# Performance work log

Hardware: AMD Instinct MI355X
Metric: run time of the kernel (lower is better)

## Reference

```python
import jax, jax.numpy as jnp
import numpy as np

D_MODEL = 1024
D_STATE = 32
EXPAND = 2
D_INNER = D_MODEL * EXPAND          # 2048
DT_RANK = D_MODEL // 16             # 64
LN_EPS = 1e-5


def setup_inputs() -> dict:
    key = jax.random.key(0)
    ks = jax.random.split(key, 9)
    s = 0.02
    x = jax.random.normal(ks[0], (2, 2048, D_MODEL), dtype=jnp.float32)
    W_in = jax.random.normal(ks[1], (2 * D_INNER, D_MODEL), dtype=jnp.float32) * s
    W_x = jax.random.normal(ks[2], (DT_RANK + 2 * D_STATE, D_INNER), dtype=jnp.float32) * s
    W_dt = jax.random.normal(ks[3], (D_INNER, DT_RANK), dtype=jnp.float32) * s
    b_dt = jax.random.normal(ks[4], (D_INNER,), dtype=jnp.float32) * s
    A_real0 = jax.random.normal(ks[5], (D_INNER, D_STATE), dtype=jnp.float32) * 0.5
    A_log_real = jnp.log(jnp.clip(-A_real0, 1e-4, None))
    A_imag = jax.random.normal(ks[6], (D_INNER, D_STATE), dtype=jnp.float32) * 0.1
    D_param = jnp.ones((D_INNER,), dtype=jnp.float32)
    W_out = jax.random.normal(ks[7], (D_MODEL, D_INNER), dtype=jnp.float32) * s
    ln_g = jnp.ones((D_MODEL,), dtype=jnp.float32)
    ln_b = jnp.zeros((D_MODEL,), dtype=jnp.float32)
    return {"x": x, "W_in": W_in, "W_x": W_x, "W_dt": W_dt, "b_dt": b_dt,
            "A_log_real": A_log_real, "A_imag": A_imag, "D_param": D_param,
            "W_out": W_out, "ln_g": ln_g, "ln_b": ln_b}


def _forward(x, W_in, W_x, W_dt, b_dt, A_log_real, A_imag, D_param, W_out, ln_g, ln_b):
    B, T, _ = x.shape
    residual = x
    # LayerNorm
    mu = jnp.mean(x, axis=-1, keepdims=True)
    var = jnp.mean((x - mu) ** 2, axis=-1, keepdims=True)
    xn = (x - mu) * jax.lax.rsqrt(var + LN_EPS) * ln_g + ln_b
    # in_proj -> (x_ssm, z)
    xz = jnp.einsum('btd,ed->bte', xn, W_in)            # (B,T,2*d_inner)
    x_ssm, z = jnp.split(xz, 2, axis=-1)
    # x_proj -> dt_low, B, C
    x_dbl = jnp.einsum('bte,re->btr', x_ssm, W_x)        # (B,T,dt_rank+2*d_state)
    dt_low = x_dbl[..., :DT_RANK]
    B_param = x_dbl[..., DT_RANK:DT_RANK + D_STATE]      # (B,T,N)
    C_param = x_dbl[..., DT_RANK + D_STATE:]             # (B,T,N)
    dt = jax.nn.softplus(jnp.einsum('btr,er->bte', dt_low, W_dt) + b_dt)  # (B,T,d_inner)
    # A = -exp(A_log_real) + i * A_imag, complex state split into (hr, hi)
    Ar = -jnp.exp(A_log_real)                             # (d_inner,N)
    Ai = A_imag

    def step(carry, inp):
        hr, hi = carry                                    # (B,d_inner,N)
        dt_t, B_t, C_t, x_t = inp                         # (B,d_inner),(B,N),(B,N),(B,d_inner)
        dtE = dt_t[:, :, None]                            # (B,d_inner,1)
        scale = jnp.exp(Ar[None] * dtE)
        ang = Ai[None] * dtE
        dAr = scale * jnp.cos(ang)
        dAi = scale * jnp.sin(ang)
        dBx = (dt_t * x_t)[:, :, None] * B_t[:, None, :]  # real input injection
        hr2 = dAr * hr - dAi * hi + dBx
        hi2 = dAr * hi + dAi * hr
        y = jnp.sum(hr2 * C_t[:, None, :], axis=-1)       # real part of (h * C).sum
        return (hr2, hi2), y

    h0 = jnp.zeros((B, D_INNER, D_STATE), dtype=x.dtype)
    xs = (jnp.transpose(dt, (1, 0, 2)), jnp.transpose(B_param, (1, 0, 2)),
          jnp.transpose(C_param, (1, 0, 2)), jnp.transpose(x_ssm, (1, 0, 2)))
    _, ys = jax.lax.scan(step, (h0, h0), xs)              # (T,B,d_inner)
    y = jnp.transpose(ys, (1, 0, 2)) + D_param * x_ssm
    y = y * jax.nn.silu(z)
    out = jnp.einsum('bte,de->btd', y, W_out)
    return residual + out  # dropout is identity at eval


def reference(x, W_in, W_x, W_dt, b_dt, A_log_real, A_imag, D_param, W_out, ln_g, ln_b):
    return _forward(x, W_in, W_x, W_dt, b_dt, A_log_real, A_imag, D_param, W_out, ln_g, ln_b)
```

## Files before the change

kernel.cpp:

```cpp
#include <hip/hip_runtime.h>
#include <math.h>

#define D_MODEL 1024
#define D_STATE 32
#define D_INNER 2048
#define DT_RANK 64
#define BT 4096
#define XZLD 4224
#define LN_EPS 1e-5f

typedef __attribute__((ext_vector_type(8))) short short8;
typedef __attribute__((ext_vector_type(4))) float f32x4;
typedef const __attribute__((address_space(1))) void* gp_t;
typedef __attribute__((address_space(3))) void* lp_t;

__device__ __forceinline__ ushort bf16r(float f) {
    unsigned u = __float_as_uint(f);
    u += 0x7fff + ((u >> 16) & 1);
    return (ushort)(u >> 16);
}

__global__ __launch_bounds__(256) void cvt_bf16(const float* __restrict__ in,
                                                ushort* __restrict__ out, int n4) {
    int i = blockIdx.x * 256 + threadIdx.x;
    if (i >= n4) return;
    float4 v = ((const float4*)in)[i];
    ushort4 o;
    o.x = bf16r(v.x); o.y = bf16r(v.y); o.z = bf16r(v.z); o.w = bf16r(v.w);
    ((ushort4*)out)[i] = o;
}

__global__ __launch_bounds__(256) void transpose_cvt(const float* __restrict__ in,
                                                     ushort* __restrict__ out) {
    __shared__ float tile[32][33];
    int bx = blockIdx.x * 32;
    int by = blockIdx.y * 32;
    int tx = threadIdx.x & 31, ty = threadIdx.x >> 5;
    #pragma unroll
    for (int i = 0; i < 32; i += 8)
        tile[ty + i][tx] = in[(size_t)(bx + ty + i) * 1024 + by + tx];
    __syncthreads();
    #pragma unroll
    for (int i = 0; i < 32; i += 8)
        out[(size_t)(by + ty + i) * 2048 + bx + tx] = bf16r(tile[tx][ty + i]);
}

__global__ __launch_bounds__(256) void ln_kernel(const float* __restrict__ x,
                                                 const float* __restrict__ g,
                                                 const float* __restrict__ b,
                                                 ushort* __restrict__ xn) {
    int row = blockIdx.x;
    const float4* xr = (const float4*)(x + (size_t)row * D_MODEL);
    float4 v = xr[threadIdx.x];
    float s  = v.x + v.y + v.z + v.w;
    float ss = v.x*v.x + v.y*v.y + v.z*v.z + v.w*v.w;
    #pragma unroll
    for (int off = 32; off > 0; off >>= 1) {
        s  += __shfl_down(s,  off, 64);
        ss += __shfl_down(ss, off, 64);
    }
    __shared__ float rs[4], rss[4];
    int wave = threadIdx.x >> 6;
    if ((threadIdx.x & 63) == 0) { rs[wave] = s; rss[wave] = ss; }
    __syncthreads();
    s  = rs[0] + rs[1] + rs[2] + rs[3];
    ss = rss[0] + rss[1] + rss[2] + rss[3];
    float mu  = s * (1.f / D_MODEL);
    float var = ss * (1.f / D_MODEL) - mu * mu;
    float inv = rsqrtf(var + LN_EPS);
    float4 gv = ((const float4*)g)[threadIdx.x];
    float4 bv = ((const float4*)b)[threadIdx.x];
    ushort4 o;
    o.x = bf16r((v.x - mu) * inv * gv.x + bv.x);
    o.y = bf16r((v.y - mu) * inv * gv.y + bv.y);
    o.z = bf16r((v.z - mu) * inv * gv.z + bv.z);
    o.w = bf16r((v.w - mu) * inv * gv.w + bv.w);
    ((ushort4*)(xn + (size_t)row * D_MODEL))[threadIdx.x] = o;
}

template<int RESID>
__global__ __launch_bounds__(256) void gemm_bt_bf16(
    const ushort* __restrict__ A, const ushort* __restrict__ B,
    float* __restrict__ C, int ldc, int K,
    const float* __restrict__ resid)
{
    __shared__ __align__(16) ushort As[128 * 32];
    __shared__ __align__(16) ushort Bs[128 * 32];
    int tid = threadIdx.x;
    int bm = blockIdx.x * 128, bn = blockIdx.y * 128;
    int wave = tid >> 6, lane = tid & 63;
    int wm = (wave & 1) * 64, wn = (wave >> 1) * 64;
    int quad = lane >> 4, m16 = lane & 15;
    int grow = tid >> 2;
    int gcol = (tid & 3) * 8;
    const size_t a0 = (size_t)(bm + grow) * K + gcol;
    const size_t b0 = (size_t)(bn + grow) * K + gcol;
    char* asw = (char*)As + wave * 1024;
    char* bsw = (char*)Bs + wave * 1024;

    f32x4 acc[4][4] = {};
    for (int k0 = 0; k0 < K; k0 += 32) {
        __builtin_amdgcn_global_load_lds((gp_t)(A + a0 + k0),                 (lp_t)asw,          16, 0, 0);
        __builtin_amdgcn_global_load_lds((gp_t)(A + a0 + (size_t)64*K + k0),  (lp_t)(asw + 4096), 16, 0, 0);
        __builtin_amdgcn_global_load_lds((gp_t)(B + b0 + k0),                 (lp_t)bsw,          16, 0, 0);
        __builtin_amdgcn_global_load_lds((gp_t)(B + b0 + (size_t)64*K + k0),  (lp_t)(bsw + 4096), 16, 0, 0);
        __syncthreads();
        short8 af[4], bf[4];
        #pragma unroll
        for (int i = 0; i < 4; ++i)
            af[i] = *(const short8*)&As[(wm + i * 16 + m16) * 32 + quad * 8];
        #pragma unroll
        for (int j = 0; j < 4; ++j)
            bf[j] = *(const short8*)&Bs[(wn + j * 16 + m16) * 32 + quad * 8];
        #pragma unroll
        for (int i = 0; i < 4; ++i)
            #pragma unroll
            for (int j = 0; j < 4; ++j)
                acc[i][j] = __builtin_amdgcn_mfma_f32_16x16x32_bf16(
                    af[i], bf[j], acc[i][j], 0, 0, 0);
        __syncthreads();
    }
    #pragma unroll
    for (int i = 0; i < 4; ++i) {
        #pragma unroll
        for (int r = 0; r < 4; ++r) {
            int row = bm + wm + i * 16 + quad * 4 + r;
            #pragma unroll
            for (int j = 0; j < 4; ++j) {
                int col = bn + wn + j * 16 + m16;
                float v = acc[i][j][r];
                if (RESID) v += resid[(size_t)row * ldc + col];
                C[(size_t)row * ldc + col] = v;
            }
        }
    }
}

template<int ACT>
__global__ __launch_bounds__(256) void gemm_nt(const float* __restrict__ A, int lda,
                                               const float* __restrict__ B, int ldb,
                                               float* __restrict__ C, int ldc,
                                               int K,
                                               const float* __restrict__ bias) {
    __shared__ float As[16][68];
    __shared__ float Bs[16][68];
    int tid = threadIdx.x;
    int bm = blockIdx.x * 64;
    int bn = blockIdx.y * 64;
    int tx = tid & 15, ty = tid >> 4;
    int lr = tid >> 2;
    int lk = (tid & 3) << 2;
    const float* Ap = A + (size_t)(bm + lr) * lda + lk;
    const float* Bp = B + (size_t)(bn + lr) * ldb + lk;
    float acc[4][4] = {};
    for (int k0 = 0; k0 < K; k0 += 16) {
        float4 a4 = *(const float4*)(Ap + k0);
        float4 b4 = *(const float4*)(Bp + k0);
        As[lk+0][lr] = a4.x; As[lk+1][lr] = a4.y; As[lk+2][lr] = a4.z; As[lk+3][lr] = a4.w;
        Bs[lk+0][lr] = b4.x; Bs[lk+1][lr] = b4.y; Bs[lk+2][lr] = b4.z; Bs[lk+3][lr] = b4.w;
        __syncthreads();
        #pragma unroll
        for (int k = 0; k < 16; ++k) {
            float4 av = *(const float4*)&As[k][ty << 2];
            float4 bv = *(const float4*)&Bs[k][tx << 2];
            float ar[4] = {av.x, av.y, av.z, av.w};
            float br[4] = {bv.x, bv.y, bv.z, bv.w};
            #pragma unroll
            for (int i = 0; i < 4; ++i)
                #pragma unroll
                for (int j = 0; j < 4; ++j)
                    acc[i][j] = fmaf(ar[i], br[j], acc[i][j]);
        }
        __syncthreads();
    }
    #pragma unroll
    for (int i = 0; i < 4; ++i) {
        int row = bm + (ty << 2) + i;
        #pragma unroll
        for (int j = 0; j < 4; ++j) {
            int col = bn + (tx << 2) + j;
            float v = acc[i][j];
            if (bias)  v += bias[col];
            if (ACT == 1) v = (v > 20.f) ? v : __logf(1.f + __expf(v));
            C[(size_t)row * ldc + col] = v;
        }
    }
}

__global__ __launch_bounds__(256) void scan_kernel(
    const float* __restrict__ xz,
    const float* __restrict__ dtm,
    const float* __restrict__ A_log_real,
    const float* __restrict__ A_imag,
    const float* __restrict__ D_param,
    ushort* __restrict__ y)
{
    const int tid = threadIdx.x;
    const int s   = tid & 31;
    const int el  = tid >> 5;
    const int b   = blockIdx.x >> 8;
    const int e0  = (blockIdx.x & 255) << 3;
    const int e   = e0 + el;
    const int stt = tid >> 3;
    const int sk  = tid & 7;
    const int btt = tid >> 4;
    const int bk  = (tid & 15) << 2;

    __shared__ __align__(16) float dxz[2][8][32][4];
    __shared__ __align__(16) float bcs[2][32][64];
    __shared__ __align__(16) float red[8][32][32];

    const float Ar   = -__expf(A_log_real[e * D_STATE + s]);
    const float Ai2p = A_imag[e * D_STATE + s] * 0.15915494f;
    const float Dp   = D_param[e];
    float hr = 0.f, hi = 0.f;
    const float* xzb = xz + (size_t)b * 2048 * XZLD;
    const float* bcb = xzb + 4096 + DT_RANK;
    const float* dtb = dtm + (size_t)b * 2048 * 2048;
    ushort*      yb  = y   + (size_t)b * 2048 * 2048;
    const int sx4 = (s & 7) << 2;

    float r_d, r_x, r_z;
    float4 r_bc0, r_bc1;
    {
        r_d = dtb[(size_t)stt * 2048 + e0 + sk];
        r_x = xzb[(size_t)stt * XZLD + e0 + sk];
        r_z = xzb[(size_t)stt * XZLD + 2048 + e0 + sk];
        r_bc0 = *(const float4*)&bcb[(size_t)btt * XZLD + bk];
        r_bc1 = *(const float4*)&bcb[(size_t)(btt + 16) * XZLD + bk];
        dxz[0][sk][stt][0] = r_d; dxz[0][sk][stt][2] = r_x; dxz[0][sk][stt][3] = r_z;
        *(float4*)&bcs[0][btt][bk]      = r_bc0;
        *(float4*)&bcs[0][btt + 16][bk] = r_bc1;
    }
    for (int c = 0; c < 64; ++c) {
        const int buf = c & 1;
        __syncthreads();
        if (c < 63) {
            const int tn = (c + 1) * 32;
            r_d = dtb[(size_t)(tn + stt) * 2048 + e0 + sk];
            r_x = xzb[(size_t)(tn + stt) * XZLD + e0 + sk];
            r_z = xzb[(size_t)(tn + stt) * XZLD + 2048 + e0 + sk];
            r_bc0 = *(const float4*)&bcb[(size_t)(tn + btt) * XZLD + bk];
            r_bc1 = *(const float4*)&bcb[(size_t)(tn + btt + 16) * XZLD + bk];
        }
        #pragma unroll 8
        for (int tt = 0; tt < 32; ++tt) {
            float4 dxv = *(const float4*)&dxz[buf][el][tt][0];
            float Bv = bcs[buf][tt][s];
            float Cv = bcs[buf][tt][32 + s];
            float dtv = dxv.x, xv = dxv.z;
            float sc = __expf(Ar * dtv);
            float u  = Ai2p * dtv;
            float sa = __builtin_amdgcn_sinf(u);
            float ca = __builtin_amdgcn_cosf(u);
            float dAr = sc * ca, dAi = sc * sa;
            float dBx = (dtv * xv) * Bv;
            float hr2 = dAr * hr - dAi * hi + dBx;
            hi = dAr * hi + dAi * hr;
            hr = hr2;
            red[el][tt][s ^ ((tt & 7) << 2)] = hr * Cv;
        }
        float acc = 0.f;
        #pragma unroll
        for (int p = 0; p < 8; ++p) {
            float4 v = *(const float4*)&red[el][s][(p << 2) ^ sx4];
            acc += (v.x + v.y) + (v.z + v.w);
        }
        float2 xzg = *(const float2*)&dxz[buf][el][s][2];
        float sig = 1.f / (1.f + __expf(-xzg.y));
        yb[(size_t)(c * 32 + s) * 2048 + e] = bf16r((acc + Dp * xzg.x) * xzg.y * sig);
        if (c < 63) {
            const int nb = buf ^ 1;
            dxz[nb][sk][stt][0] = r_d; dxz[nb][sk][stt][2] = r_x; dxz[nb][sk][stt][3] = r_z;
            *(float4*)&bcs[nb][btt][bk]      = r_bc0;
            *(float4*)&bcs[nb][btt + 16][bk] = r_bc1;
        }
    }
}

extern "C" void kernel_launch(void* const* d_in, const int* in_sizes, int n_in,
                              void* d_out, int out_size, void* d_ws, size_t ws_size,
                              hipStream_t stream) {
    const float* x          = (const float*)d_in[0];
    const float* W_in       = (const float*)d_in[1];
    const float* W_x        = (const float*)d_in[2];
    const float* W_dt       = (const float*)d_in[3];
    const float* b_dt       = (const float*)d_in[4];
    const float* A_log_real = (const float*)d_in[5];
    const float* A_imag     = (const float*)d_in[6];
    const float* D_param    = (const float*)d_in[7];
    const float* W_out      = (const float*)d_in[8];
    const float* ln_g       = (const float*)d_in[9];
    const float* ln_b       = (const float*)d_in[10];
    float* out = (float*)d_out;

    char* ws = (char*)d_ws;
    float*  xz      = (float*) (ws);
    float*  dt      = (float*) (ws + ((size_t) 66 << 20));
    ushort* xn_bf   = (ushort*)(ws + ((size_t) 98 << 20));
    ushort* Waug    = (ushort*)(ws + ((size_t)106 << 20));
    ushort* y_bf    = (ushort*)(ws + ((size_t)115 << 20));
    ushort* Wout_bf = (ushort*)(ws + ((size_t)131 << 20));
    float*  Wcomb   = (float*) (ws);
    ushort* Wx_bf   = (ushort*)(ws + ((size_t)  1 << 20));
    ushort* WinT_bf = (ushort*)(ws + ((size_t)  2 << 20));

    cvt_bf16<<<4096, 256, 0, stream>>>(W_in,  Waug,    4096*1024/4);
    cvt_bf16<<<2048, 256, 0, stream>>>(W_out, Wout_bf, 1024*2048/4);
    cvt_bf16<<< 256, 256, 0, stream>>>(W_x,   Wx_bf,    128*2048/4);
    transpose_cvt<<<dim3(64, 32), 256, 0, stream>>>(W_in, WinT_bf);
    gemm_bt_bf16<0><<<dim3(1, 8), 256, 0, stream>>>(
        Wx_bf, WinT_bf, Wcomb, 1024, 2048, nullptr);
    cvt_bf16<<<128, 256, 0, stream>>>(Wcomb, Waug + (size_t)4096*1024, 128*1024/4);
    ln_kernel<<<BT, 256, 0, stream>>>(x, ln_g, ln_b, xn_bf);
    gemm_bt_bf16<0><<<dim3(BT/128, XZLD/128), 256, 0, stream>>>(
        xn_bf, Waug, xz, XZLD, D_MODEL, nullptr);
    gemm_nt<1><<<dim3(BT/64, D_INNER/64), 256, 0, stream>>>(
        xz + 4096, XZLD, W_dt, DT_RANK, dt, D_INNER, DT_RANK, b_dt);
    scan_kernel<<<512, 256, 0, stream>>>(xz, dt, A_log_real, A_imag, D_param, y_bf);
    gemm_bt_bf16<1><<<dim3(BT/128, D_MODEL/128), 256, 0, stream>>>(
        y_bf, Wout_bf, out, D_MODEL, D_INNER, x);
}
```

Measured before the change: 509.7 us.

## Move dt projection to bf16 MFMA GEMM and restructure scan reduction with DPP

Replaces the fp32 scalar dt-projection GEMM with the bf16 MFMA GEMM, adding a softplus+bias epilogue, a bf16 conversion of dt_low and of W_dt. The scan kernel now precomputes dt*x, D*x and silu(z) once per chunk in shared memory. It processes two timesteps per iteration, uses exp2 with a prescaled A, and swaps the shared-memory transposed reduction over states for DPP cross-lane reductions. Extra kernel launches and bf16 rounding of dt_low add small cost and some precision loss.

```diff
diff --git a/kernel.cpp b/kernel.cpp
--- a/kernel.cpp
+++ b/kernel.cpp
@@ -20,11 +20,36 @@
     return (ushort)(u >> 16);
 }
 
+__device__ __forceinline__ float dpp_red32(float x) {
+    int t;
+    t = __builtin_amdgcn_update_dpp(0, __float_as_int(x), 0x111, 0xf, 0xf, true);
+    x += __int_as_float(t);
+    t = __builtin_amdgcn_update_dpp(0, __float_as_int(x), 0x112, 0xf, 0xf, true);
+    x += __int_as_float(t);
+    t = __builtin_amdgcn_update_dpp(0, __float_as_int(x), 0x114, 0xf, 0xf, true);
+    x += __int_as_float(t);
+    t = __builtin_amdgcn_update_dpp(0, __float_as_int(x), 0x118, 0xf, 0xf, true);
+    x += __int_as_float(t);
+    t = __builtin_amdgcn_update_dpp(0, __float_as_int(x), 0x142, 0xa, 0xf, true);
+    x += __int_as_float(t);
+    return x;
+}
+
 __global__ __launch_bounds__(256) void cvt_bf16(const float* __restrict__ in,
                                                 ushort* __restrict__ out, int n4) {
     int i = blockIdx.x * 256 + threadIdx.x;
     if (i >= n4) return;
     float4 v = ((const float4*)in)[i];
+    ushort4 o;
+    o.x = bf16r(v.x); o.y = bf16r(v.y); o.z = bf16r(v.z); o.w = bf16r(v.w);
+    ((ushort4*)out)[i] = o;
+}
+
+__global__ __launch_bounds__(256) void cvt_dtlow(const float* __restrict__ xz,
+                                                 ushort* __restrict__ out) {
+    int i = blockIdx.x * 256 + threadIdx.x;
+    int row = i >> 4, c = (i & 15) << 2;
+    float4 v = *(const float4*)&xz[(size_t)row * XZLD + 4096 + c];
     ushort4 o;
     o.x = bf16r(v.x); o.y = bf16r(v.y); o.z = bf16r(v.z); o.w = bf16r(v.w);
     ((ushort4*)out)[i] = o;
@@ -78,11 +103,11 @@
     ((ushort4*)(xn + (size_t)row * D_MODEL))[threadIdx.x] = o;
 }
 
-template<int RESID>
+template<int RESID, int ACT>
 __global__ __launch_bounds__(256) void gemm_bt_bf16(
     const ushort* __restrict__ A, const ushort* __restrict__ B,
     float* __restrict__ C, int ldc, int K,
-    const float* __restrict__ resid)
+    const float* __restrict__ resid, const float* __restrict__ bias)
 {
     __shared__ __align__(16) ushort As[128 * 32];
     __shared__ __align__(16) ushort Bs[128 * 32];
@@ -129,60 +154,13 @@
             for (int j = 0; j < 4; ++j) {
                 int col = bn + wn + j * 16 + m16;
                 float v = acc[i][j][r];
+                if (ACT == 1) {
+                    v += bias[col];
+                    v = (v > 20.f) ? v : __logf(1.f + __expf(v));
+                }
                 if (RESID) v += resid[(size_t)row * ldc + col];
                 C[(size_t)row * ldc + col] = v;
             }
-        }
-    }
-}
-
-template<int ACT>
-__global__ __launch_bounds__(256) void gemm_nt(const float* __restrict__ A, int lda,
-                                               const float* __restrict__ B, int ldb,
-                                               float* __restrict__ C, int ldc,
-                                               int K,
-                                               const float* __restrict__ bias) {
-    __shared__ float As[16][68];
-    __shared__ float Bs[16][68];
-    int tid = threadIdx.x;
-    int bm = blockIdx.x * 64;
-    int bn = blockIdx.y * 64;
-    int tx = tid & 15, ty = tid >> 4;
-    int lr = tid >> 2;
-    int lk = (tid & 3) << 2;
-    const float* Ap = A + (size_t)(bm + lr) * lda + lk;
-    const float* Bp = B + (size_t)(bn + lr) * ldb + lk;
-    float acc[4][4] = {};
-    for (int k0 = 0; k0 < K; k0 += 16) {
-        float4 a4 = *(const float4*)(Ap + k0);
-        float4 b4 = *(const float4*)(Bp + k0);
-        As[lk+0][lr] = a4.x; As[lk+1][lr] = a4.y; As[lk+2][lr] = a4.z; As[lk+3][lr] = a4.w;
-        Bs[lk+0][lr] = b4.x; Bs[lk+1][lr] = b4.y; Bs[lk+2][lr] = b4.z; Bs[lk+3][lr] = b4.w;
-        __syncthreads();
-        #pragma unroll
-        for (int k = 0; k < 16; ++k) {
-            float4 av = *(const float4*)&As[k][ty << 2];
-            float4 bv = *(const float4*)&Bs[k][tx << 2];
-            float ar[4] = {av.x, av.y, av.z, av.w};
-            float br[4] = {bv.x, bv.y, bv.z, bv.w};
-            #pragma unroll
-            for (int i = 0; i < 4; ++i)
-                #pragma unroll
-                for (int j = 0; j < 4; ++j)
-                    acc[i][j] = fmaf(ar[i], br[j], acc[i][j]);
-        }
-        __syncthreads();
-    }
-    #pragma unroll
-    for (int i = 0; i < 4; ++i) {
-        int row = bm + (ty << 2) + i;
-        #pragma unroll
-        for (int j = 0; j < 4; ++j) {
-            int col = bn + (tx << 2) + j;
-            float v = acc[i][j];
-            if (bias)  v += bias[col];
-            if (ACT == 1) v = (v > 20.f) ? v : __logf(1.f + __expf(v));
-            C[(size_t)row * ldc + col] = v;
         }
     }
 }
@@ -195,42 +173,47 @@
     const float* __restrict__ D_param,
     ushort* __restrict__ y)
 {
-    const int tid = threadIdx.x;
-    const int s   = tid & 31;
-    const int el  = tid >> 5;
-    const int b   = blockIdx.x >> 8;
-    const int e0  = (blockIdx.x & 255) << 3;
-    const int e   = e0 + el;
-    const int stt = tid >> 3;
-    const int sk  = tid & 7;
-    const int btt = tid >> 4;
-    const int bk  = (tid & 15) << 2;
-
-    __shared__ __align__(16) float dxz[2][8][32][4];
-    __shared__ __align__(16) float bcs[2][32][64];
-    __shared__ __align__(16) float red[8][32][32];
-
-    const float Ar   = -__expf(A_log_real[e * D_STATE + s]);
+    const int tid  = threadIdx.x;
+    const int s    = tid & 31;
+    const int el   = tid >> 5;
+    const int b    = blockIdx.x >> 8;
+    const int e0   = (blockIdx.x & 255) << 3;
+    const int e    = e0 + el;
+    const int sk   = tid & 7;
+    const int stt  = tid >> 3;
+    const int brow = tid >> 4;
+    const int bcp  = tid & 15;
+
+    __shared__ __align__(16) float dxp[2][8][17][4];
+    __shared__ __align__(16) float xzs[2][8][34][2];
+    __shared__ __align__(16) float bcs[2][32][68];
+
+    const float Ar2  = -__expf(A_log_real[e * D_STATE + s]) * 1.44269504f;
     const float Ai2p = A_imag[e * D_STATE + s] * 0.15915494f;
-    const float Dp   = D_param[e];
+    const float Dps  = D_param[e0 + sk];
     float hr = 0.f, hi = 0.f;
     const float* xzb = xz + (size_t)b * 2048 * XZLD;
     const float* bcb = xzb + 4096 + DT_RANK;
     const float* dtb = dtm + (size_t)b * 2048 * 2048;
     ushort*      yb  = y   + (size_t)b * 2048 * 2048;
-    const int sx4 = (s & 7) << 2;
 
     float r_d, r_x, r_z;
-    float4 r_bc0, r_bc1;
+    float2 rb0, rc0, rb1, rc1;
     {
         r_d = dtb[(size_t)stt * 2048 + e0 + sk];
         r_x = xzb[(size_t)stt * XZLD + e0 + sk];
         r_z = xzb[(size_t)stt * XZLD + 2048 + e0 + sk];
-        r_bc0 = *(const float4*)&bcb[(size_t)btt * XZLD + bk];
-        r_bc1 = *(const float4*)&bcb[(size_t)(btt + 16) * XZLD + bk];
-        dxz[0][sk][stt][0] = r_d; dxz[0][sk][stt][2] = r_x; dxz[0][sk][stt][3] = r_z;
-        *(float4*)&bcs[0][btt][bk]      = r_bc0;
-        *(float4*)&bcs[0][btt + 16][bk] = r_bc1;
+        rb0 = *(const float2*)&bcb[(size_t)brow * XZLD + 2 * bcp];
+        rc0 = *(const float2*)&bcb[(size_t)brow * XZLD + 32 + 2 * bcp];
+        rb1 = *(const float2*)&bcb[(size_t)(brow + 16) * XZLD + 2 * bcp];
+        rc1 = *(const float2*)&bcb[(size_t)(brow + 16) * XZLD + 32 + 2 * bcp];
+        float dtx = r_d * r_x;
+        float g   = r_z / (1.f + __expf(-r_z));
+        float Dx  = Dps * r_x;
+        *(float2*)&dxp[0][sk][stt >> 1][(stt & 1) * 2] = make_float2(r_d, dtx);
+        *(float2*)&xzs[0][sk][stt]                     = make_float2(Dx, g);
+        *(float4*)&bcs[0][brow][4 * bcp]      = make_float4(rb0.x, rc0.x, rb0.y, rc0.y);
+        *(float4*)&bcs[0][brow + 16][4 * bcp] = make_float4(rb1.x, rc1.x, rb1.y, rc1.y);
     }
     for (int c = 0; c < 64; ++c) {
         const int buf = c & 1;
@@ -240,40 +223,47 @@
             r_d = dtb[(size_t)(tn + stt) * 2048 + e0 + sk];
             r_x = xzb[(size_t)(tn + stt) * XZLD + e0 + sk];
             r_z = xzb[(size_t)(tn + stt) * XZLD + 2048 + e0 + sk];
-            r_bc0 = *(const float4*)&bcb[(size_t)(tn + btt) * XZLD + bk];
-            r_bc1 = *(const float4*)&bcb[(size_t)(tn + btt + 16) * XZLD + bk];
+            rb0 = *(const float2*)&bcb[(size_t)(tn + brow) * XZLD + 2 * bcp];
+            rc0 = *(const float2*)&bcb[(size_t)(tn + brow) * XZLD + 32 + 2 * bcp];
+            rb1 = *(const float2*)&bcb[(size_t)(tn + brow + 16) * XZLD + 2 * bcp];
+            rc1 = *(const float2*)&bcb[(size_t)(tn + brow + 16) * XZLD + 32 + 2 * bcp];
         }
-        #pragma unroll 8
-        for (int tt = 0; tt < 32; ++tt) {
-            float4 dxv = *(const float4*)&dxz[buf][el][tt][0];
-            float Bv = bcs[buf][tt][s];
-            float Cv = bcs[buf][tt][32 + s];
-            float dtv = dxv.x, xv = dxv.z;
-            float sc = __expf(Ar * dtv);
-            float u  = Ai2p * dtv;
-            float sa = __builtin_amdgcn_sinf(u);
-            float ca = __builtin_amdgcn_cosf(u);
+        #pragma unroll 4
+        for (int tp = 0; tp < 16; ++tp) {
+            float4 dd  = *(const float4*)&dxp[buf][el][tp][0];
+            float2 bc0 = *(const float2*)&bcs[buf][2 * tp][2 * s];
+            float2 bc1 = *(const float2*)&bcs[buf][2 * tp + 1][2 * s];
+            float sc = __builtin_amdgcn_exp2f(Ar2 * dd.x);
+            float u  = Ai2p * dd.x;
+            float sa = __builtin_amdgcn_sinf(u), ca = __builtin_amdgcn_cosf(u);
             float dAr = sc * ca, dAi = sc * sa;
-            float dBx = (dtv * xv) * Bv;
-            float hr2 = dAr * hr - dAi * hi + dBx;
-            hi = dAr * hi + dAi * hr;
-            hr = hr2;
-            red[el][tt][s ^ ((tt & 7) << 2)] = hr * Cv;
+            float hrn = fmaf(dAr, hr, fmaf(-dAi, hi, dd.y * bc0.x));
+            hi = fmaf(dAr, hi, dAi * hr); hr = hrn;
+            float p0 = hr * bc0.y;
+            sc = __builtin_amdgcn_exp2f(Ar2 * dd.z);
+            u  = Ai2p * dd.z;
+            sa = __builtin_amdgcn_sinf(u); ca = __builtin_amdgcn_cosf(u);
+            dAr = sc * ca; dAi = sc * sa;
+            hrn = fmaf(dAr, hr, fmaf(-dAi, hi, dd.w * bc1.x));
+            hi = fmaf(dAr, hi, dAi * hr); hr = hrn;
+            float p1 = hr * bc1.y;
+            p0 = dpp_red32(p0);
+            p1 = dpp_red32(p1);
+            if (s == 31) {
+                float4 xg = *(const float4*)&xzs[buf][el][2 * tp];
+                yb[(size_t)(c * 32 + 2 * tp) * 2048 + e]     = bf16r((p0 + xg.x) * xg.y);
+                yb[(size_t)(c * 32 + 2 * tp + 1) * 2048 + e] = bf16r((p1 + xg.z) * xg.w);
+            }
         }
-        float acc = 0.f;
-        #pragma unroll
-        for (int p = 0; p < 8; ++p) {
-            float4 v = *(const float4*)&red[el][s][(p << 2) ^ sx4];
-            acc += (v.x + v.y) + (v.z + v.w);
-        }
-        float2 xzg = *(const float2*)&dxz[buf][el][s][2];
-        float sig = 1.f / (1.f + __expf(-xzg.y));
-        yb[(size_t)(c * 32 + s) * 2048 + e] = bf16r((acc + Dp * xzg.x) * xzg.y * sig);
         if (c < 63) {
             const int nb = buf ^ 1;
-            dxz[nb][sk][stt][0] = r_d; dxz[nb][sk][stt][2] = r_x; dxz[nb][sk][stt][3] = r_z;
-            *(float4*)&bcs[nb][btt][bk]      = r_bc0;
-            *(float4*)&bcs[nb][btt + 16][bk] = r_bc1;
+            float dtx = r_d * r_x;
+            float g   = r_z / (1.f + __expf(-r_z));
+            float Dx  = Dps * r_x;
+            *(float2*)&dxp[nb][sk][stt >> 1][(stt & 1) * 2] = make_float2(r_d, dtx);
+            *(float2*)&xzs[nb][sk][stt]                     = make_float2(Dx, g);
+            *(float4*)&bcs[nb][brow][4 * bcp]      = make_float4(rb0.x, rc0.x, rb0.y, rc0.y);
+            *(float4*)&bcs[nb][brow + 16][4 * bcp] = make_float4(rb1.x, rc1.x, rb1.y, rc1.y);
         }
     }
 }
@@ -295,12 +285,14 @@
     float* out = (float*)d_out;
 
     char* ws = (char*)d_ws;
-    float*  xz      = (float*) (ws);
-    float*  dt      = (float*) (ws + ((size_t) 66 << 20));
-    ushort* xn_bf   = (ushort*)(ws + ((size_t) 98 << 20));
-    ushort* Waug    = (ushort*)(ws + ((size_t)106 << 20));
-    ushort* y_bf    = (ushort*)(ws + ((size_t)115 << 20));
-    ushort* Wout_bf = (ushort*)(ws + ((size_t)131 << 20));
+    float*  xz       = (float*) (ws);
+    float*  dt       = (float*) (ws + ((size_t) 66 << 20));
+    ushort* xn_bf    = (ushort*)(ws + ((size_t) 98 << 20));
+    ushort* Waug     = (ushort*)(ws + ((size_t)106 << 20));
+    ushort* y_bf     = (ushort*)(ws + ((size_t)115 << 20));
+    ushort* Wout_bf  = (ushort*)(ws + ((size_t)131 << 20));
+    ushort* Wdt_bf   = (ushort*)(ws + ((size_t)135 << 20));
+    ushort* dtlow_bf = (ushort*)(ws + ((size_t)136 << 20));
     float*  Wcomb   = (float*) (ws);
     ushort* Wx_bf   = (ushort*)(ws + ((size_t)  1 << 20));
     ushort* WinT_bf = (ushort*)(ws + ((size_t)  2 << 20));
@@ -308,16 +300,18 @@
     cvt_bf16<<<4096, 256, 0, stream>>>(W_in,  Waug,    4096*1024/4);
     cvt_bf16<<<2048, 256, 0, stream>>>(W_out, Wout_bf, 1024*2048/4);
     cvt_bf16<<< 256, 256, 0, stream>>>(W_x,   Wx_bf,    128*2048/4);
+    cvt_bf16<<< 128, 256, 0, stream>>>(W_dt,  Wdt_bf,   2048*64/4);
     transpose_cvt<<<dim3(64, 32), 256, 0, stream>>>(W_in, WinT_bf);
-    gemm_bt_bf16<0><<<dim3(1, 8), 256, 0, stream>>>(
-        Wx_bf, WinT_bf, Wcomb, 1024, 2048, nullptr);
+    gemm_bt_bf16<0,0><<<dim3(1, 8), 256, 0, stream>>>(
+        Wx_bf, WinT_bf, Wcomb, 1024, 2048, nullptr, nullptr);
     cvt_bf16<<<128, 256, 0, stream>>>(Wcomb, Waug + (size_t)4096*1024, 128*1024/4);
     ln_kernel<<<BT, 256, 0, stream>>>(x, ln_g, ln_b, xn_bf);
-    gemm_bt_bf16<0><<<dim3(BT/128, XZLD/128), 256, 0, stream>>>(
-        xn_bf, Waug, xz, XZLD, D_MODEL, nullptr);
-    gemm_nt<1><<<dim3(BT/64, D_INNER/64), 256, 0, stream>>>(
-        xz + 4096, XZLD, W_dt, DT_RANK, dt, D_INNER, DT_RANK, b_dt);
+    gemm_bt_bf16<0,0><<<dim3(BT/128, XZLD/128), 256, 0, stream>>>(
+        xn_bf, Waug, xz, XZLD, D_MODEL, nullptr, nullptr);
+    cvt_dtlow<<<256, 256, 0, stream>>>(xz, dtlow_bf);
+    gemm_bt_bf16<0,1><<<dim3(BT/128, D_INNER/128), 256, 0, stream>>>(
+        dtlow_bf, Wdt_bf, dt, D_INNER, DT_RANK, nullptr, b_dt);
     scan_kernel<<<512, 256, 0, stream>>>(xz, dt, A_log_real, A_imag, D_param, y_bf);
-    gemm_bt_bf16<1><<<dim3(BT/128, D_MODEL/128), 256, 0, stream>>>(
-        y_bf, Wout_bf, out, D_MODEL, D_INNER, x);
-}
+    gemm_bt_bf16<1,0><<<dim3(BT/128, D_MODEL/128), 256, 0, stream>>>(
+        y_bf, Wout_bf, out, D_MODEL, D_INNER, x, nullptr);
+}
```

New measurement: 552.2 us. 8.3% more time.
